# Kernel tuning notes

Measured on AMD Instinct MI355X. Metric: run time of the kernel, lower is better.

Reference implementation:

```python
import jax, jax.numpy as jnp
import numpy as np

B, S, H, NH = 2, 2048, 768, 12
HD = H // NH  # 64
MAXPOS = 2048


def _rope_tables(max_pos, d):
    # bert4torch get_sinusoid_encoding_table: even cols sin, odd cols cos
    pos = np.arange(max_pos, dtype=np.float32)[:, None]
    div = np.exp(np.arange(0, d, 2, dtype=np.float32) * (-np.log(10000.0) / d))
    tab = np.zeros((max_pos, d), np.float32)
    tab[:, 0::2] = np.sin(pos * div)
    tab[:, 1::2] = np.cos(pos * div)
    cos = np.concatenate([tab[:, 1::2], tab[:, 1::2]], axis=1)  # [:,1::2].repeat(1,2)
    sin = np.concatenate([tab[:, 0::2], tab[:, 0::2]], axis=1)  # [:,0::2].repeat(1,2)
    return jnp.asarray(cos), jnp.asarray(sin)


def setup_inputs() -> dict:
    key = jax.random.key(0)
    ks = jax.random.split(key, 10)
    s = 0.02
    inp = {}
    inp["hidden_states"] = jax.random.normal(ks[0], (B, S, H), jnp.float32)
    inp["attention_mask"] = jnp.ones((B, 1, 1, S), jnp.float32)
    for i, n in enumerate(["q", "k", "v", "o"]):
        inp[f"W{n}"] = (jax.random.normal(ks[1 + i], (H, H), jnp.float32) * s)
        inp[f"b{n}"] = jnp.zeros((H,), jnp.float32)
    cos, sin = _rope_tables(MAXPOS, HD)
    inp["cos_position"] = cos
    inp["sin_position"] = sin
    return inp


def _apply_rope(qw, cos, sin):
    # Faithful to source: seq_len_dim defaults to 1, which on a
    # [B, heads, S, head_dim] tensor is the HEADS axis.
    L = qw.shape[1]
    qw2 = jnp.concatenate([-qw[..., 1::2], qw[..., 0::2]], axis=-1)
    return qw * cos[:L][None, :, None, :] + qw2 * sin[:L][None, :, None, :]


def reference(hidden_states, attention_mask, Wq, bq, Wk, bk, Wv, bv, Wo, bo,
              cos_position, sin_position):
    b, s, _ = hidden_states.shape

    def heads(x):  # [b,s,H] -> [b,NH,s,HD]
        return x.reshape(b, s, NH, HD).transpose(0, 2, 1, 3)

    q = heads(hidden_states @ Wq + bq)
    k = heads(hidden_states @ Wk + bk)
    v = heads(hidden_states @ Wv + bv)
    q = _apply_rope(q, cos_position, sin_position)
    k = _apply_rope(k, cos_position, sin_position)
    scores = jnp.einsum('bnid,bnjd->bnij', q, k) / jnp.sqrt(jnp.float32(HD))
    scores = scores + (1.0 - attention_mask) * (-10000.0)
    probs = jax.nn.softmax(scores, axis=-1)  # dropout is identity in eval
    ctx = jnp.einsum('bnij,bnjd->bnid', probs, v)
    ctx = ctx.transpose(0, 2, 1, 3).reshape(b, s, H)
    return ctx @ Wo + bo
```

## Files before the change

### kernel.cpp

```cpp
#include <hip/hip_runtime.h>

#define B 2
#define S 2048
#define H 768
#define NH 12
#define HD 64
#define BS (B * S)
#define LOG2E 1.4426950408889634f

typedef unsigned short u16;
typedef short short8 __attribute__((ext_vector_type(8)));
typedef float f32x4 __attribute__((ext_vector_type(4)));

__device__ __forceinline__ u16 f2bf(float f) {
    union { float f; unsigned u; } c; c.f = f;
    unsigned u = c.u + 0x7FFFu + ((c.u >> 16) & 1u);
    return (u16)(u >> 16);
}
__device__ __forceinline__ float bf2f(u16 h) {
    union { unsigned u; float f; } c; c.u = ((unsigned)h) << 16;
    return c.f;
}

__device__ __forceinline__ void g2l16(const u16* g, u16* l) {
    __builtin_amdgcn_global_load_lds(
        (const __attribute__((address_space(1))) void*)g,
        (__attribute__((address_space(3))) void*)l, 16, 0, 0);
}

__global__ __launch_bounds__(256) void prep_hs_kernel(
    const float* __restrict__ src, u16* __restrict__ dst)
{
    size_t i = ((size_t)blockIdx.x * 256 + threadIdx.x) * 8;
    float4 a = *(const float4*)(src + i);
    float4 b = *(const float4*)(src + i + 4);
    short8 p;
    p[0] = (short)f2bf(a.x); p[1] = (short)f2bf(a.y);
    p[2] = (short)f2bf(a.z); p[3] = (short)f2bf(a.w);
    p[4] = (short)f2bf(b.x); p[5] = (short)f2bf(b.y);
    p[6] = (short)f2bf(b.z); p[7] = (short)f2bf(b.w);
    *(short8*)(dst + i) = p;
}

__global__ __launch_bounds__(256) void prep_w_kernel(
    const float* __restrict__ Wq, const float* __restrict__ Wk,
    const float* __restrict__ Wv, const float* __restrict__ Wo,
    u16* __restrict__ WTqkv, u16* __restrict__ WTo)
{
    __shared__ float Lt[64 * 65];
    const int t = threadIdx.x;
    const int z = blockIdx.z;
    const float* W = (z == 0) ? Wq : (z == 1) ? Wk : (z == 2) ? Wv : Wo;
    u16* D = (z == 3) ? WTo : (WTqkv + (size_t)z * H * H);
    const int k0 = blockIdx.x * 64, n0 = blockIdx.y * 64;

    #pragma unroll
    for (int u = 0; u < 4; ++u) {
        int f = t + u * 256;
        int r = f >> 4, c4 = (f & 15) * 4;
        float4 w = *(const float4*)(W + (size_t)(k0 + r) * H + n0 + c4);
        Lt[r * 65 + c4 + 0] = w.x; Lt[r * 65 + c4 + 1] = w.y;
        Lt[r * 65 + c4 + 2] = w.z; Lt[r * 65 + c4 + 3] = w.w;
    }
    __syncthreads();
    #pragma unroll
    for (int u = 0; u < 4; ++u) {
        int f = t + u * 256;
        int n = f >> 4, k4 = (f & 15) * 4;
        ushort4 p;
        p.x = f2bf(Lt[(k4 + 0) * 65 + n]);
        p.y = f2bf(Lt[(k4 + 1) * 65 + n]);
        p.z = f2bf(Lt[(k4 + 2) * 65 + n]);
        p.w = f2bf(Lt[(k4 + 3) * 65 + n]);
        *(ushort4*)(D + (size_t)(n0 + n) * H + k0 + k4) = p;
    }
}

__global__ __launch_bounds__(256) void gemm_qkv_kernel(
    const u16* __restrict__ A, const u16* __restrict__ BT,
    const float* __restrict__ bq, const float* __restrict__ bk,
    const float* __restrict__ bv,
    u16* __restrict__ Qb, u16* __restrict__ Kb, u16* __restrict__ VT)
{
    __shared__ alignas(16) u16 As[128 * 72];
    __shared__ alignas(16) u16 Bs[128 * 72];

    const int tid  = threadIdx.x;
    const int w    = tid >> 6;
    const int lane = tid & 63;
    const int quad = lane >> 4;
    const int l15  = lane & 15;
    const int wm = (w & 1) * 64, wn = (w >> 1) * 64;
    const int m0 = blockIdx.x * 128;
    const int n0 = blockIdx.y * 128;
    const int lr = tid >> 3, lc8 = (tid & 7) * 8;

    f32x4 acc[4][4];
    #pragma unroll
    for (int i = 0; i < 4; ++i)
        #pragma unroll
        for (int j = 0; j < 4; ++j) acc[i][j] = (f32x4){0.f, 0.f, 0.f, 0.f};

    short8 pa[2], pb[2], pa2[2], pb2[2];
    #pragma unroll
    for (int u = 0; u < 2; ++u) {
        pa[u]  = *(const short8*)(A  + (size_t)(m0 + lr + u * 32) * H + lc8);
        pb[u]  = *(const short8*)(BT + (size_t)(n0 + lr + u * 32) * H + lc8);
        pa2[u] = *(const short8*)(A  + (size_t)(m0 + lr + 64 + u * 32) * H + lc8);
        pb2[u] = *(const short8*)(BT + (size_t)(n0 + lr + 64 + u * 32) * H + lc8);
    }

    for (int k0 = 0; k0 < H; k0 += 64) {
        __syncthreads();
        #pragma unroll
        for (int u = 0; u < 2; ++u) {
            *(short8*)&As[(lr + u * 32) * 72 + lc8] = pa[u];
            *(short8*)&Bs[(lr + u * 32) * 72 + lc8] = pb[u];
            *(short8*)&As[(lr + 64 + u * 32) * 72 + lc8] = pa2[u];
            *(short8*)&Bs[(lr + 64 + u * 32) * 72 + lc8] = pb2[u];
        }
        if (k0 + 64 < H) {
            #pragma unroll
            for (int u = 0; u < 2; ++u) {
                pa[u]  = *(const short8*)(A  + (size_t)(m0 + lr + u * 32) * H + k0 + 64 + lc8);
                pb[u]  = *(const short8*)(BT + (size_t)(n0 + lr + u * 32) * H + k0 + 64 + lc8);
                pa2[u] = *(const short8*)(A  + (size_t)(m0 + lr + 64 + u * 32) * H + k0 + 64 + lc8);
                pb2[u] = *(const short8*)(BT + (size_t)(n0 + lr + 64 + u * 32) * H + k0 + 64 + lc8);
            }
        }
        __syncthreads();
        #pragma unroll
        for (int kc = 0; kc < 64; kc += 32) {
            short8 af[4], bf[4];
            #pragma unroll
            for (int mi = 0; mi < 4; ++mi)
                af[mi] = *(const short8*)&As[(wm + mi * 16 + l15) * 72 + kc + quad * 8];
            #pragma unroll
            for (int ni = 0; ni < 4; ++ni)
                bf[ni] = *(const short8*)&Bs[(wn + ni * 16 + l15) * 72 + kc + quad * 8];
            #pragma unroll
            for (int mi = 0; mi < 4; ++mi)
                #pragma unroll
                for (int ni = 0; ni < 4; ++ni)
                    acc[mi][ni] = __builtin_amdgcn_mfma_f32_16x16x32_bf16(
                        af[mi], bf[ni], acc[mi][ni], 0, 0, 0);
        }
    }

    #pragma unroll
    for (int mi = 0; mi < 4; ++mi) {
        const int mbase = m0 + wm + mi * 16 + quad * 4;
        #pragma unroll
        for (int ni = 0; ni < 4; ++ni) {
            const int col = n0 + wn + ni * 16 + l15;
            const int which = col / H;
            const int c = col - which * H;
            const int h = c >> 6, d = c & 63;
            if (which == 2) {
                const float bias = bv[c];
                const int b_ = mbase >> 11, s = mbase & (S - 1);
                ushort4 pk;
                pk.x = f2bf(acc[mi][ni][0] + bias);
                pk.y = f2bf(acc[mi][ni][1] + bias);
                pk.z = f2bf(acc[mi][ni][2] + bias);
                pk.w = f2bf(acc[mi][ni][3] + bias);
                *(ushort4*)&VT[(((size_t)b_ * NH + h) * HD + d) * S + s] = pk;
            } else {
                u16* dst = (which == 0) ? Qb : Kb;
                const float bias = (which == 0) ? bq[c] : bk[c];
                #pragma unroll
                for (int r = 0; r < 4; ++r) {
                    int m = mbase + r;
                    int b_ = m >> 11, s = m & (S - 1);
                    dst[(((size_t)b_ * NH + h) * S + s) * HD + d] =
                        f2bf(acc[mi][ni][r] + bias);
                }
            }
        }
    }
}

__global__ __launch_bounds__(256) void gemm_out_kernel(
    const u16* __restrict__ A, const u16* __restrict__ BT,
    const float* __restrict__ bo, float* __restrict__ out)
{
    __shared__ alignas(16) u16 As[128 * 72];
    __shared__ alignas(16) u16 Bs[128 * 72];

    const int tid  = threadIdx.x;
    const int w    = tid >> 6;
    const int lane = tid & 63;
    const int quad = lane >> 4;
    const int l15  = lane & 15;
    const int wm = (w & 1) * 64, wn = (w >> 1) * 64;
    const int m0 = blockIdx.x * 128;
    const int n0 = blockIdx.y * 128;
    const int lr = tid >> 3, lc8 = (tid & 7) * 8;

    f32x4 acc[4][4];
    #pragma unroll
    for (int i = 0; i < 4; ++i)
        #pragma unroll
        for (int j = 0; j < 4; ++j) acc[i][j] = (f32x4){0.f, 0.f, 0.f, 0.f};

    short8 pa[2], pb[2], pa2[2], pb2[2];
    #pragma unroll
    for (int u = 0; u < 2; ++u) {
        pa[u]  = *(const short8*)(A  + (size_t)(m0 + lr + u * 32) * H + lc8);
        pb[u]  = *(const short8*)(BT + (size_t)(n0 + lr + u * 32) * H + lc8);
        pa2[u] = *(const short8*)(A  + (size_t)(m0 + lr + 64 + u * 32) * H + lc8);
        pb2[u] = *(const short8*)(BT + (size_t)(n0 + lr + 64 + u * 32) * H + lc8);
    }

    for (int k0 = 0; k0 < H; k0 += 64) {
        __syncthreads();
        #pragma unroll
        for (int u = 0; u < 2; ++u) {
            *(short8*)&As[(lr + u * 32) * 72 + lc8] = pa[u];
            *(short8*)&Bs[(lr + u * 32) * 72 + lc8] = pb[u];
            *(short8*)&As[(lr + 64 + u * 32) * 72 + lc8] = pa2[u];
            *(short8*)&Bs[(lr + 64 + u * 32) * 72 + lc8] = pb2[u];
        }
        if (k0 + 64 < H) {
            #pragma unroll
            for (int u = 0; u < 2; ++u) {
                pa[u]  = *(const short8*)(A  + (size_t)(m0 + lr + u * 32) * H + k0 + 64 + lc8);
                pb[u]  = *(const short8*)(BT + (size_t)(n0 + lr + u * 32) * H + k0 + 64 + lc8);
                pa2[u] = *(const short8*)(A  + (size_t)(m0 + lr + 64 + u * 32) * H + k0 + 64 + lc8);
                pb2[u] = *(const short8*)(BT + (size_t)(n0 + lr + 64 + u * 32) * H + k0 + 64 + lc8);
            }
        }
        __syncthreads();
        #pragma unroll
        for (int kc = 0; kc < 64; kc += 32) {
            short8 af[4], bf[4];
            #pragma unroll
            for (int mi = 0; mi < 4; ++mi)
                af[mi] = *(const short8*)&As[(wm + mi * 16 + l15) * 72 + kc + quad * 8];
            #pragma unroll
            for (int ni = 0; ni < 4; ++ni)
                bf[ni] = *(const short8*)&Bs[(wn + ni * 16 + l15) * 72 + kc + quad * 8];
            #pragma unroll
            for (int mi = 0; mi < 4; ++mi)
                #pragma unroll
                for (int ni = 0; ni < 4; ++ni)
                    acc[mi][ni] = __builtin_amdgcn_mfma_f32_16x16x32_bf16(
                        af[mi], bf[ni], acc[mi][ni], 0, 0, 0);
        }
    }

    #pragma unroll
    for (int mi = 0; mi < 4; ++mi) {
        const int mbase = m0 + wm + mi * 16 + quad * 4;
        #pragma unroll
        for (int ni = 0; ni < 4; ++ni) {
            const int col = n0 + wn + ni * 16 + l15;
            const float bias = bo[col];
            #pragma unroll
            for (int r = 0; r < 4; ++r)
                out[(size_t)(mbase + r) * H + col] = acc[mi][ni][r] + bias;
        }
    }
}

__global__ __launch_bounds__(256) void rope_kernel(
    u16* __restrict__ Qb, u16* __restrict__ Kb,
    const float* __restrict__ cosp, const float* __restrict__ sinp)
{
    int row  = blockIdx.x * 4 + (threadIdx.x >> 6);
    int lane = threadIdx.x & 63;
    u16* X = (blockIdx.y == 0) ? Qb : Kb;
    const float scale = (blockIdx.y == 0) ? (0.125f * LOG2E) : 1.0f;
    int n = (row / S) % NH;
    float x = bf2f(X[(size_t)row * HD + lane]);
    int p = (lane < 32) ? (2 * lane + 1) : (2 * (lane - 32));
    float xp = __shfl(x, p, 64);
    float x2 = (lane < 32) ? -xp : xp;
    float c  = cosp[n * HD + lane];
    float sn = sinp[n * HD + lane];
    X[(size_t)row * HD + lane] = f2bf(fmaf(x, c, x2 * sn) * scale);
}

__global__ __launch_bounds__(256) void attn_mfma_kernel(
    const u16* __restrict__ Q, const u16* __restrict__ K,
    const u16* __restrict__ VT, const float* __restrict__ mask,
    u16* __restrict__ ctx)
{
    __shared__ alignas(16) u16 Kbuf[2][64 * 64];
    __shared__ alignas(16) u16 Vbuf[2][64 * 64];
    __shared__ alignas(16) u16 Ps[4 * 16 * 72];
    __shared__ float mt[S];

    const int tid  = threadIdx.x;
    const int w    = tid >> 6;
    const int lane = tid & 63;
    const int quad = lane >> 4;
    const int l15  = lane & 15;
    const int bn = blockIdx.y, b = bn / NH, hh = bn % NH;
    const int q0 = blockIdx.x * 64;
    const int NT = S / 64;

    {
        const float* mb = mask + (size_t)b * S;
        #pragma unroll
        for (int u = 0; u < 2; ++u) {
            int j = (tid + u * 256) * 4;
            float4 mv = *(const float4*)(mb + j);
            mt[j + 0] = (1.0f - mv.x) * (-10000.0f * LOG2E);
            mt[j + 1] = (1.0f - mv.y) * (-10000.0f * LOG2E);
            mt[j + 2] = (1.0f - mv.z) * (-10000.0f * LOG2E);
            mt[j + 3] = (1.0f - mv.w) * (-10000.0f * LOG2E);
        }
    }

    const u16* Qp = Q + ((size_t)bn * S + q0 + w * 16 + l15) * HD + quad * 8;
    const short8 qa0 = *(const short8*)(Qp);
    const short8 qa1 = *(const short8*)(Qp + 32);

    const u16* Kb = K + (size_t)bn * S * HD;
    const u16* Vb = VT + (size_t)bn * HD * S;

    int srow[2], slc[2];
    #pragma unroll
    for (int u = 0; u < 2; ++u) {
        int s = u * 256 + tid;
        srow[u] = s >> 3;
        slc[u]  = (s & 7) ^ (srow[u] & 7);
    }

    #define STAGE(JT, NB)                                                     \
        _Pragma("unroll")                                                     \
        for (int u = 0; u < 2; ++u) {                                         \
            g2l16(Kb + (size_t)((JT) * 64 + srow[u]) * HD + slc[u] * 8,       \
                  &Kbuf[NB][(u * 256 + w * 64) * 8]);                         \
            g2l16(Vb + (size_t)srow[u] * S + (JT) * 64 + slc[u] * 8,          \
                  &Vbuf[NB][(u * 256 + w * 64) * 8]);                         \
        }

    STAGE(0, 0)

    f32x4 o[4];
    float l_p[4];
    #pragma unroll
    for (int n = 0; n < 4; ++n) o[n] = (f32x4){0.f, 0.f, 0.f, 0.f};
    #pragma unroll
    for (int r = 0; r < 4; ++r) l_p[r] = 0.f;

    for (int jt = 0; jt < NT; ++jt) {
        const int cur = jt & 1;
        __syncthreads();
        if (jt + 1 < NT) { STAGE(jt + 1, cur ^ 1) }

        const u16* Kc = Kbuf[cur];
        const u16* Vc = Vbuf[cur];

        f32x4 sc[4];
        #pragma unroll
        for (int n = 0; n < 4; ++n) {
            const int row = n * 16 + l15, sw = row & 7;
            const short8 kb0 = *(const short8*)&Kc[row * 64 + ((quad) ^ sw) * 8];
            const short8 kb1 = *(const short8*)&Kc[row * 64 + ((quad + 4) ^ sw) * 8];
            f32x4 a = (f32x4){0.f, 0.f, 0.f, 0.f};
            a = __builtin_amdgcn_mfma_f32_16x16x32_bf16(qa0, kb0, a, 0, 0, 0);
            a = __builtin_amdgcn_mfma_f32_16x16x32_bf16(qa1, kb1, a, 0, 0, 0);
            sc[n] = a;
        }

        short8 vf[8];
        #pragma unroll
        for (int n = 0; n < 4; ++n) {
            const int row = n * 16 + l15, sw = row & 7;
            vf[n * 2 + 0] = *(const short8*)&Vc[row * 64 + ((quad) ^ sw) * 8];
            vf[n * 2 + 1] = *(const short8*)&Vc[row * 64 + ((quad + 4) ^ sw) * 8];
        }

        #pragma unroll
        for (int n = 0; n < 4; ++n) {
            const float mtn = mt[jt * 64 + n * 16 + l15];
            #pragma unroll
            for (int r = 0; r < 4; ++r) {
                float p = __builtin_amdgcn_exp2f(sc[n][r] + mtn);
                l_p[r] += p;
                Ps[w * 1152 + (quad * 4 + r) * 72 + n * 16 + l15] = f2bf(p);
            }
        }

        asm volatile("s_waitcnt lgkmcnt(0)" ::: "memory");

        const u16* Pw = &Ps[w * 1152 + l15 * 72 + quad * 8];
        const short8 pa0 = *(const short8*)(Pw);
        const short8 pa1 = *(const short8*)(Pw + 32);
        #pragma unroll
        for (int n = 0; n < 4; ++n) {
            o[n] = __builtin_amdgcn_mfma_f32_16x16x32_bf16(pa0, vf[n * 2 + 0], o[n], 0, 0, 0);
            o[n] = __builtin_amdgcn_mfma_f32_16x16x32_bf16(pa1, vf[n * 2 + 1], o[n], 0, 0, 0);
        }
    }
    #undef STAGE

    #pragma unroll
    for (int r = 0; r < 4; ++r) {
        float l = l_p[r];
        #pragma unroll
        for (int off = 8; off >= 1; off >>= 1)
            l += __shfl_xor(l, off, 16);
        float inv = 1.0f / l;
        int s = q0 + w * 16 + quad * 4 + r;
        #pragma unroll
        for (int n = 0; n < 4; ++n)
            ctx[((size_t)b * S + s) * H + hh * 64 + n * 16 + l15] =
                f2bf(o[n][r] * inv);
    }
}

extern "C" void kernel_launch(void* const* d_in, const int* in_sizes, int n_in,
                              void* d_out, int out_size, void* d_ws, size_t ws_size,
                              hipStream_t stream)
{
    const float* hs   = (const float*)d_in[0];
    const float* mask = (const float*)d_in[1];
    const float* Wq   = (const float*)d_in[2];
    const float* bq   = (const float*)d_in[3];
    const float* Wk   = (const float*)d_in[4];
    const float* bk   = (const float*)d_in[5];
    const float* Wv   = (const float*)d_in[6];
    const float* bv   = (const float*)d_in[7];
    const float* Wo   = (const float*)d_in[8];
    const float* bo   = (const float*)d_in[9];
    const float* cosp = (const float*)d_in[10];
    const float* sinp = (const float*)d_in[11];
    float* out = (float*)d_out;

    const size_t per = (size_t)B * NH * S * HD;
    u16* ws    = (u16*)d_ws;
    u16* hsb   = ws;
    u16* WTqkv = hsb + per;
    u16* WTo   = WTqkv + (size_t)3 * H * H;
    u16* Qb    = WTo + (size_t)H * H;
    u16* Kb    = Qb + per;
    u16* VT    = Kb + per;
    u16* ctxb  = VT + per;

    prep_hs_kernel<<<(BS * H) / 2048, 256, 0, stream>>>(hs, hsb);
    prep_w_kernel<<<dim3(12, 12, 4), 256, 0, stream>>>(
        Wq, Wk, Wv, Wo, WTqkv, WTo);

    gemm_qkv_kernel<<<dim3(BS / 128, 2304 / 128), 256, 0, stream>>>(
        hsb, WTqkv, bq, bk, bv, Qb, Kb, VT);

    rope_kernel<<<dim3(B * NH * S / 4, 2), 256, 0, stream>>>(
        Qb, Kb, cosp, sinp);

    attn_mfma_kernel<<<dim3(S / 64, B * NH), 256, 0, stream>>>(
        Qb, Kb, VT, mask, ctxb);

    gemm_out_kernel<<<dim3(BS / 128, H / 128), 256, 0, stream>>>(
        ctxb, WTo, bo, out);
}
```

Measured before the change: 206.8 us.

## Use 2 waves with 32 query rows each in attention; halve output GEMM N tile

```diff
diff --git a/kernel.cpp b/kernel.cpp
--- a/kernel.cpp
+++ b/kernel.cpp
@@ -185,31 +185,30 @@
     const float* __restrict__ bo, float* __restrict__ out)
 {
     __shared__ alignas(16) u16 As[128 * 72];
-    __shared__ alignas(16) u16 Bs[128 * 72];
+    __shared__ alignas(16) u16 Bs[64 * 72];
 
     const int tid  = threadIdx.x;
     const int w    = tid >> 6;
     const int lane = tid & 63;
     const int quad = lane >> 4;
     const int l15  = lane & 15;
-    const int wm = (w & 1) * 64, wn = (w >> 1) * 64;
+    const int wm = (w & 1) * 64, wn = (w >> 1) * 32;
     const int m0 = blockIdx.x * 128;
-    const int n0 = blockIdx.y * 128;
+    const int n0 = blockIdx.y * 64;
     const int lr = tid >> 3, lc8 = (tid & 7) * 8;
 
-    f32x4 acc[4][4];
+    f32x4 acc[4][2];
     #pragma unroll
     for (int i = 0; i < 4; ++i)
         #pragma unroll
-        for (int j = 0; j < 4; ++j) acc[i][j] = (f32x4){0.f, 0.f, 0.f, 0.f};
-
-    short8 pa[2], pb[2], pa2[2], pb2[2];
+        for (int j = 0; j < 2; ++j) acc[i][j] = (f32x4){0.f, 0.f, 0.f, 0.f};
+
+    short8 pa[2], pa2[2], pb[2];
     #pragma unroll
     for (int u = 0; u < 2; ++u) {
         pa[u]  = *(const short8*)(A  + (size_t)(m0 + lr + u * 32) * H + lc8);
+        pa2[u] = *(const short8*)(A  + (size_t)(m0 + lr + 64 + u * 32) * H + lc8);
         pb[u]  = *(const short8*)(BT + (size_t)(n0 + lr + u * 32) * H + lc8);
-        pa2[u] = *(const short8*)(A  + (size_t)(m0 + lr + 64 + u * 32) * H + lc8);
-        pb2[u] = *(const short8*)(BT + (size_t)(n0 + lr + 64 + u * 32) * H + lc8);
     }
 
     for (int k0 = 0; k0 < H; k0 += 64) {
@@ -217,33 +216,31 @@
         #pragma unroll
         for (int u = 0; u < 2; ++u) {
             *(short8*)&As[(lr + u * 32) * 72 + lc8] = pa[u];
+            *(short8*)&As[(lr + 64 + u * 32) * 72 + lc8] = pa2[u];
             *(short8*)&Bs[(lr + u * 32) * 72 + lc8] = pb[u];
-            *(short8*)&As[(lr + 64 + u * 32) * 72 + lc8] = pa2[u];
-            *(short8*)&Bs[(lr + 64 + u * 32) * 72 + lc8] = pb2[u];
         }
         if (k0 + 64 < H) {
             #pragma unroll
             for (int u = 0; u < 2; ++u) {
                 pa[u]  = *(const short8*)(A  + (size_t)(m0 + lr + u * 32) * H + k0 + 64 + lc8);
+                pa2[u] = *(const short8*)(A  + (size_t)(m0 + lr + 64 + u * 32) * H + k0 + 64 + lc8);
                 pb[u]  = *(const short8*)(BT + (size_t)(n0 + lr + u * 32) * H + k0 + 64 + lc8);
-                pa2[u] = *(const short8*)(A  + (size_t)(m0 + lr + 64 + u * 32) * H + k0 + 64 + lc8);
-                pb2[u] = *(const short8*)(BT + (size_t)(n0 + lr + 64 + u * 32) * H + k0 + 64 + lc8);
             }
         }
         __syncthreads();
         #pragma unroll
         for (int kc = 0; kc < 64; kc += 32) {
-            short8 af[4], bf[4];
+            short8 af[4], bf[2];
             #pragma unroll
             for (int mi = 0; mi < 4; ++mi)
                 af[mi] = *(const short8*)&As[(wm + mi * 16 + l15) * 72 + kc + quad * 8];
             #pragma unroll
-            for (int ni = 0; ni < 4; ++ni)
+            for (int ni = 0; ni < 2; ++ni)
                 bf[ni] = *(const short8*)&Bs[(wn + ni * 16 + l15) * 72 + kc + quad * 8];
             #pragma unroll
             for (int mi = 0; mi < 4; ++mi)
                 #pragma unroll
-                for (int ni = 0; ni < 4; ++ni)
+                for (int ni = 0; ni < 2; ++ni)
                     acc[mi][ni] = __builtin_amdgcn_mfma_f32_16x16x32_bf16(
                         af[mi], bf[ni], acc[mi][ni], 0, 0, 0);
         }
@@ -253,7 +250,7 @@
     for (int mi = 0; mi < 4; ++mi) {
         const int mbase = m0 + wm + mi * 16 + quad * 4;
         #pragma unroll
-        for (int ni = 0; ni < 4; ++ni) {
+        for (int ni = 0; ni < 2; ++ni) {
             const int col = n0 + wn + ni * 16 + l15;
             const float bias = bo[col];
             #pragma unroll
@@ -281,14 +278,14 @@
     X[(size_t)row * HD + lane] = f2bf(fmaf(x, c, x2 * sn) * scale);
 }
 
-__global__ __launch_bounds__(256) void attn_mfma_kernel(
+__global__ __launch_bounds__(128) void attn_mfma_kernel(
     const u16* __restrict__ Q, const u16* __restrict__ K,
     const u16* __restrict__ VT, const float* __restrict__ mask,
     u16* __restrict__ ctx)
 {
     __shared__ alignas(16) u16 Kbuf[2][64 * 64];
     __shared__ alignas(16) u16 Vbuf[2][64 * 64];
-    __shared__ alignas(16) u16 Ps[4 * 16 * 72];
+    __shared__ alignas(16) u16 Ps[2 * 32 * 72];
     __shared__ float mt[S];
 
     const int tid  = threadIdx.x;
@@ -303,8 +300,8 @@
     {
         const float* mb = mask + (size_t)b * S;
         #pragma unroll
-        for (int u = 0; u < 2; ++u) {
-            int j = (tid + u * 256) * 4;
+        for (int u = 0; u < 4; ++u) {
+            int j = (u * 128 + tid) * 4;
             float4 mv = *(const float4*)(mb + j);
             mt[j + 0] = (1.0f - mv.x) * (-10000.0f * LOG2E);
             mt[j + 1] = (1.0f - mv.y) * (-10000.0f * LOG2E);
@@ -313,38 +310,46 @@
         }
     }
 
-    const u16* Qp = Q + ((size_t)bn * S + q0 + w * 16 + l15) * HD + quad * 8;
-    const short8 qa0 = *(const short8*)(Qp);
-    const short8 qa1 = *(const short8*)(Qp + 32);
+    short8 qa[2][2];
+    #pragma unroll
+    for (int t = 0; t < 2; ++t) {
+        const u16* Qp =
+            Q + ((size_t)bn * S + q0 + w * 32 + t * 16 + l15) * HD + quad * 8;
+        qa[t][0] = *(const short8*)(Qp);
+        qa[t][1] = *(const short8*)(Qp + 32);
+    }
 
     const u16* Kb = K + (size_t)bn * S * HD;
     const u16* Vb = VT + (size_t)bn * HD * S;
 
-    int srow[2], slc[2];
-    #pragma unroll
-    for (int u = 0; u < 2; ++u) {
-        int s = u * 256 + tid;
+    int srow[4], slc[4];
+    #pragma unroll
+    for (int u = 0; u < 4; ++u) {
+        int s = u * 128 + tid;
         srow[u] = s >> 3;
         slc[u]  = (s & 7) ^ (srow[u] & 7);
     }
 
     #define STAGE(JT, NB)                                                     \
         _Pragma("unroll")                                                     \
-        for (int u = 0; u < 2; ++u) {                                         \
+        for (int u = 0; u < 4; ++u) {                                         \
             g2l16(Kb + (size_t)((JT) * 64 + srow[u]) * HD + slc[u] * 8,       \
-                  &Kbuf[NB][(u * 256 + w * 64) * 8]);                         \
+                  &Kbuf[NB][(u * 128 + w * 64) * 8]);                         \
             g2l16(Vb + (size_t)srow[u] * S + (JT) * 64 + slc[u] * 8,          \
-                  &Vbuf[NB][(u * 256 + w * 64) * 8]);                         \
+                  &Vbuf[NB][(u * 128 + w * 64) * 8]);                         \
         }
 
     STAGE(0, 0)
 
-    f32x4 o[4];
-    float l_p[4];
-    #pragma unroll
-    for (int n = 0; n < 4; ++n) o[n] = (f32x4){0.f, 0.f, 0.f, 0.f};
-    #pragma unroll
-    for (int r = 0; r < 4; ++r) l_p[r] = 0.f;
+    f32x4 o[2][4];
+    float l_p[2][4];
+    #pragma unroll
+    for (int t = 0; t < 2; ++t)
+        #pragma unroll
+        for (int n = 0; n < 4; ++n) {
+            o[t][n] = (f32x4){0.f, 0.f, 0.f, 0.f};
+            l_p[t][n] = 0.f;
+        }
 
     for (int jt = 0; jt < NT; ++jt) {
         const int cur = jt & 1;
@@ -354,63 +359,79 @@
         const u16* Kc = Kbuf[cur];
         const u16* Vc = Vbuf[cur];
 
-        f32x4 sc[4];
+        f32x4 sc[2][4];
         #pragma unroll
         for (int n = 0; n < 4; ++n) {
             const int row = n * 16 + l15, sw = row & 7;
             const short8 kb0 = *(const short8*)&Kc[row * 64 + ((quad) ^ sw) * 8];
             const short8 kb1 = *(const short8*)&Kc[row * 64 + ((quad + 4) ^ sw) * 8];
-            f32x4 a = (f32x4){0.f, 0.f, 0.f, 0.f};
-            a = __builtin_amdgcn_mfma_f32_16x16x32_bf16(qa0, kb0, a, 0, 0, 0);
-            a = __builtin_amdgcn_mfma_f32_16x16x32_bf16(qa1, kb1, a, 0, 0, 0);
-            sc[n] = a;
-        }
-
-        short8 vf[8];
+            #pragma unroll
+            for (int t = 0; t < 2; ++t) {
+                f32x4 a = (f32x4){0.f, 0.f, 0.f, 0.f};
+                a = __builtin_amdgcn_mfma_f32_16x16x32_bf16(qa[t][0], kb0, a, 0, 0, 0);
+                a = __builtin_amdgcn_mfma_f32_16x16x32_bf16(qa[t][1], kb1, a, 0, 0, 0);
+                sc[t][n] = a;
+            }
+        }
+
+        short8 vf[4][2];
         #pragma unroll
         for (int n = 0; n < 4; ++n) {
             const int row = n * 16 + l15, sw = row & 7;
-            vf[n * 2 + 0] = *(const short8*)&Vc[row * 64 + ((quad) ^ sw) * 8];
-            vf[n * 2 + 1] = *(const short8*)&Vc[row * 64 + ((quad + 4) ^ sw) * 8];
+            vf[n][0] = *(const short8*)&Vc[row * 64 + ((quad) ^ sw) * 8];
+            vf[n][1] = *(const short8*)&Vc[row * 64 + ((quad + 4) ^ sw) * 8];
         }
 
         #pragma unroll
         for (int n = 0; n < 4; ++n) {
             const float mtn = mt[jt * 64 + n * 16 + l15];
             #pragma unroll
-            for (int r = 0; r < 4; ++r) {
-                float p = __builtin_amdgcn_exp2f(sc[n][r] + mtn);
-                l_p[r] += p;
-                Ps[w * 1152 + (quad * 4 + r) * 72 + n * 16 + l15] = f2bf(p);
+            for (int t = 0; t < 2; ++t)
+                #pragma unroll
+                for (int r = 0; r < 4; ++r) {
+                    float p = __builtin_amdgcn_exp2f(sc[t][n][r] + mtn);
+                    l_p[t][r] += p;
+                    Ps[w * 2304 + (t * 16 + quad * 4 + r) * 72 + n * 16 + l15] =
+                        f2bf(p);
+                }
+        }
+
+        asm volatile("s_waitcnt lgkmcnt(0)" ::: "memory");
+
+        short8 pa[2][2];
+        #pragma unroll
+        for (int t = 0; t < 2; ++t) {
+            const u16* Pw = &Ps[w * 2304 + (t * 16 + l15) * 72 + quad * 8];
+            pa[t][0] = *(const short8*)(Pw);
+            pa[t][1] = *(const short8*)(Pw + 32);
+        }
+        #pragma unroll
+        for (int n = 0; n < 4; ++n)
+            #pragma unroll
+            for (int t = 0; t < 2; ++t) {
+                o[t][n] = __builtin_amdgcn_mfma_f32_16x16x32_bf16(
+                    pa[t][0], vf[n][0], o[t][n], 0, 0, 0);
+                o[t][n] = __builtin_amdgcn_mfma_f32_16x16x32_bf16(
+                    pa[t][1], vf[n][1], o[t][n], 0, 0, 0);
             }
-        }
-
-        asm volatile("s_waitcnt lgkmcnt(0)" ::: "memory");
-
-        const u16* Pw = &Ps[w * 1152 + l15 * 72 + quad * 8];
-        const short8 pa0 = *(const short8*)(Pw);
-        const short8 pa1 = *(const short8*)(Pw + 32);
-        #pragma unroll
-        for (int n = 0; n < 4; ++n) {
-            o[n] = __builtin_amdgcn_mfma_f32_16x16x32_bf16(pa0, vf[n * 2 + 0], o[n], 0, 0, 0);
-            o[n] = __builtin_amdgcn_mfma_f32_16x16x32_bf16(pa1, vf[n * 2 + 1], o[n], 0, 0, 0);
-        }
     }
     #undef STAGE
 
     #pragma unroll
-    for (int r = 0; r < 4; ++r) {
-        float l = l_p[r];
-        #pragma unroll
-        for (int off = 8; off >= 1; off >>= 1)
-            l += __shfl_xor(l, off, 16);
-        float inv = 1.0f / l;
-        int s = q0 + w * 16 + quad * 4 + r;
-        #pragma unroll
-        for (int n = 0; n < 4; ++n)
-            ctx[((size_t)b * S + s) * H + hh * 64 + n * 16 + l15] =
-                f2bf(o[n][r] * inv);
-    }
+    for (int t = 0; t < 2; ++t)
+        #pragma unroll
+        for (int r = 0; r < 4; ++r) {
+            float l = l_p[t][r];
+            #pragma unroll
+            for (int off = 8; off >= 1; off >>= 1)
+                l += __shfl_xor(l, off, 16);
+            float inv = 1.0f / l;
+            int s = q0 + w * 32 + t * 16 + quad * 4 + r;
+            #pragma unroll
+            for (int n = 0; n < 4; ++n)
+                ctx[((size_t)b * S + s) * H + hh * 64 + n * 16 + l15] =
+                    f2bf(o[t][n][r] * inv);
+        }
 }
 
 extern "C" void kernel_launch(void* const* d_in, const int* in_sizes, int n_in,
@@ -451,9 +472,9 @@
     rope_kernel<<<dim3(B * NH * S / 4, 2), 256, 0, stream>>>(
         Qb, Kb, cosp, sinp);
 
-    attn_mfma_kernel<<<dim3(S / 64, B * NH), 256, 0, stream>>>(
+    attn_mfma_kernel<<<dim3(S / 64, B * NH), 128, 0, stream>>>(
         Qb, Kb, VT, mask, ctxb);
 
-    gemm_out_kernel<<<dim3(BS / 128, H / 128), 256, 0, stream>>>(
+    gemm_out_kernel<<<dim3(BS / 128, H / 64), 256, 0, stream>>>(
         ctxb, WTo, bo, out);
 }
```

Result: slower. 217.3 us (+5.1%).

## Use 32x32 MFMA with split-K waves in attention; halve output GEMM N tile

Applied to the files above, without the earlier changes.

```diff
diff --git a/kernel.cpp b/kernel.cpp
--- a/kernel.cpp
+++ b/kernel.cpp
@@ -11,6 +11,7 @@
 typedef unsigned short u16;
 typedef short short8 __attribute__((ext_vector_type(8)));
 typedef float f32x4 __attribute__((ext_vector_type(4)));
+typedef float f32x16 __attribute__((ext_vector_type(16)));
 
 __device__ __forceinline__ u16 f2bf(float f) {
     union { float f; unsigned u; } c; c.f = f;
@@ -20,6 +21,12 @@
 __device__ __forceinline__ float bf2f(u16 h) {
     union { unsigned u; float f; } c; c.u = ((unsigned)h) << 16;
     return c.f;
+}
+__device__ __forceinline__ f32x16 zero16() {
+    f32x16 v;
+    #pragma unroll
+    for (int i = 0; i < 16; ++i) v[i] = 0.f;
+    return v;
 }
 
 __device__ __forceinline__ void g2l16(const u16* g, u16* l) {
@@ -185,31 +192,30 @@
     const float* __restrict__ bo, float* __restrict__ out)
 {
     __shared__ alignas(16) u16 As[128 * 72];
-    __shared__ alignas(16) u16 Bs[128 * 72];
+    __shared__ alignas(16) u16 Bs[64 * 72];
 
     const int tid  = threadIdx.x;
     const int w    = tid >> 6;
     const int lane = tid & 63;
     const int quad = lane >> 4;
     const int l15  = lane & 15;
-    const int wm = (w & 1) * 64, wn = (w >> 1) * 64;
+    const int wm = (w & 1) * 64, wn = (w >> 1) * 32;
     const int m0 = blockIdx.x * 128;
-    const int n0 = blockIdx.y * 128;
+    const int n0 = blockIdx.y * 64;
     const int lr = tid >> 3, lc8 = (tid & 7) * 8;
 
-    f32x4 acc[4][4];
+    f32x4 acc[4][2];
     #pragma unroll
     for (int i = 0; i < 4; ++i)
         #pragma unroll
-        for (int j = 0; j < 4; ++j) acc[i][j] = (f32x4){0.f, 0.f, 0.f, 0.f};
-
-    short8 pa[2], pb[2], pa2[2], pb2[2];
+        for (int j = 0; j < 2; ++j) acc[i][j] = (f32x4){0.f, 0.f, 0.f, 0.f};
+
+    short8 pa[2], pa2[2], pb[2];
     #pragma unroll
     for (int u = 0; u < 2; ++u) {
         pa[u]  = *(const short8*)(A  + (size_t)(m0 + lr + u * 32) * H + lc8);
+        pa2[u] = *(const short8*)(A  + (size_t)(m0 + lr + 64 + u * 32) * H + lc8);
         pb[u]  = *(const short8*)(BT + (size_t)(n0 + lr + u * 32) * H + lc8);
-        pa2[u] = *(const short8*)(A  + (size_t)(m0 + lr + 64 + u * 32) * H + lc8);
-        pb2[u] = *(const short8*)(BT + (size_t)(n0 + lr + 64 + u * 32) * H + lc8);
     }
 
     for (int k0 = 0; k0 < H; k0 += 64) {
@@ -217,33 +223,31 @@
         #pragma unroll
         for (int u = 0; u < 2; ++u) {
             *(short8*)&As[(lr + u * 32) * 72 + lc8] = pa[u];
+            *(short8*)&As[(lr + 64 + u * 32) * 72 + lc8] = pa2[u];
             *(short8*)&Bs[(lr + u * 32) * 72 + lc8] = pb[u];
-            *(short8*)&As[(lr + 64 + u * 32) * 72 + lc8] = pa2[u];
-            *(short8*)&Bs[(lr + 64 + u * 32) * 72 + lc8] = pb2[u];
         }
         if (k0 + 64 < H) {
             #pragma unroll
             for (int u = 0; u < 2; ++u) {
                 pa[u]  = *(const short8*)(A  + (size_t)(m0 + lr + u * 32) * H + k0 + 64 + lc8);
+                pa2[u] = *(const short8*)(A  + (size_t)(m0 + lr + 64 + u * 32) * H + k0 + 64 + lc8);
                 pb[u]  = *(const short8*)(BT + (size_t)(n0 + lr + u * 32) * H + k0 + 64 + lc8);
-                pa2[u] = *(const short8*)(A  + (size_t)(m0 + lr + 64 + u * 32) * H + k0 + 64 + lc8);
-                pb2[u] = *(const short8*)(BT + (size_t)(n0 + lr + 64 + u * 32) * H + k0 + 64 + lc8);
             }
         }
         __syncthreads();
         #pragma unroll
         for (int kc = 0; kc < 64; kc += 32) {
-            short8 af[4], bf[4];
+            short8 af[4], bf[2];
             #pragma unroll
             for (int mi = 0; mi < 4; ++mi)
                 af[mi] = *(const short8*)&As[(wm + mi * 16 + l15) * 72 + kc + quad * 8];
             #pragma unroll
-            for (int ni = 0; ni < 4; ++ni)
+            for (int ni = 0; ni < 2; ++ni)
                 bf[ni] = *(const short8*)&Bs[(wn + ni * 16 + l15) * 72 + kc + quad * 8];
             #pragma unroll
             for (int mi = 0; mi < 4; ++mi)
                 #pragma unroll
-                for (int ni = 0; ni < 4; ++ni)
+                for (int ni = 0; ni < 2; ++ni)
                     acc[mi][ni] = __builtin_amdgcn_mfma_f32_16x16x32_bf16(
                         af[mi], bf[ni], acc[mi][ni], 0, 0, 0);
         }
@@ -253,7 +257,7 @@
     for (int mi = 0; mi < 4; ++mi) {
         const int mbase = m0 + wm + mi * 16 + quad * 4;
         #pragma unroll
-        for (int ni = 0; ni < 4; ++ni) {
+        for (int ni = 0; ni < 2; ++ni) {
             const int col = n0 + wn + ni * 16 + l15;
             const float bias = bo[col];
             #pragma unroll
@@ -286,39 +290,33 @@
     const u16* __restrict__ VT, const float* __restrict__ mask,
     u16* __restrict__ ctx)
 {
-    __shared__ alignas(16) u16 Kbuf[2][64 * 64];
-    __shared__ alignas(16) u16 Vbuf[2][64 * 64];
-    __shared__ alignas(16) u16 Ps[4 * 16 * 72];
-    __shared__ float mt[S];
+    __shared__ alignas(16) u16 smem[21504];
+    u16* const Kbase = smem;
+    u16* const Vbase = smem + 8192;
+    u16* const Psw   = smem + 16384 + (threadIdx.x >> 6) * 1280;
 
     const int tid  = threadIdx.x;
     const int w    = tid >> 6;
     const int lane = tid & 63;
-    const int quad = lane >> 4;
-    const int l15  = lane & 15;
+    const int l31  = lane & 31;
+    const int h5   = lane >> 5;
+    const int rh   = w & 1;
+    const int kh   = w >> 1;
     const int bn = blockIdx.y, b = bn / NH, hh = bn % NH;
     const int q0 = blockIdx.x * 64;
     const int NT = S / 64;
 
+    short8 qa[4];
     {
-        const float* mb = mask + (size_t)b * S;
-        #pragma unroll
-        for (int u = 0; u < 2; ++u) {
-            int j = (tid + u * 256) * 4;
-            float4 mv = *(const float4*)(mb + j);
-            mt[j + 0] = (1.0f - mv.x) * (-10000.0f * LOG2E);
-            mt[j + 1] = (1.0f - mv.y) * (-10000.0f * LOG2E);
-            mt[j + 2] = (1.0f - mv.z) * (-10000.0f * LOG2E);
-            mt[j + 3] = (1.0f - mv.w) * (-10000.0f * LOG2E);
-        }
-    }
-
-    const u16* Qp = Q + ((size_t)bn * S + q0 + w * 16 + l15) * HD + quad * 8;
-    const short8 qa0 = *(const short8*)(Qp);
-    const short8 qa1 = *(const short8*)(Qp + 32);
-
-    const u16* Kb = K + (size_t)bn * S * HD;
-    const u16* Vb = VT + (size_t)bn * HD * S;
+        const u16* Qp = Q + ((size_t)bn * S + q0 + rh * 32 + l31) * HD + h5 * 8;
+        #pragma unroll
+        for (int kc = 0; kc < 4; ++kc)
+            qa[kc] = *(const short8*)(Qp + kc * 16);
+    }
+
+    const u16* Kg = K + (size_t)bn * S * HD;
+    const u16* Vg = VT + (size_t)bn * HD * S;
+    const float* mrow = mask + (size_t)b * S;
 
     int srow[2], slc[2];
     #pragma unroll
@@ -331,85 +329,107 @@
     #define STAGE(JT, NB)                                                     \
         _Pragma("unroll")                                                     \
         for (int u = 0; u < 2; ++u) {                                         \
-            g2l16(Kb + (size_t)((JT) * 64 + srow[u]) * HD + slc[u] * 8,       \
-                  &Kbuf[NB][(u * 256 + w * 64) * 8]);                         \
-            g2l16(Vb + (size_t)srow[u] * S + (JT) * 64 + slc[u] * 8,          \
-                  &Vbuf[NB][(u * 256 + w * 64) * 8]);                         \
+            g2l16(Kg + (size_t)((JT) * 64 + srow[u]) * HD + slc[u] * 8,       \
+                  Kbase + (NB) * 4096 + (u * 256 + w * 64) * 8);              \
+            g2l16(Vg + (size_t)srow[u] * S + (JT) * 64 + slc[u] * 8,          \
+                  Vbase + (NB) * 4096 + (u * 256 + w * 64) * 8);              \
         }
 
     STAGE(0, 0)
 
-    f32x4 o[4];
-    float l_p[4];
-    #pragma unroll
-    for (int n = 0; n < 4; ++n) o[n] = (f32x4){0.f, 0.f, 0.f, 0.f};
-    #pragma unroll
-    for (int r = 0; r < 4; ++r) l_p[r] = 0.f;
+    f32x16 o0 = zero16(), o1 = zero16();
+    float l_p[16];
+    #pragma unroll
+    for (int i = 0; i < 16; ++i) l_p[i] = 0.f;
 
     for (int jt = 0; jt < NT; ++jt) {
         const int cur = jt & 1;
+        const float mv = mrow[jt * 64 + kh * 32 + l31];
         __syncthreads();
         if (jt + 1 < NT) { STAGE(jt + 1, cur ^ 1) }
 
-        const u16* Kc = Kbuf[cur];
-        const u16* Vc = Vbuf[cur];
-
-        f32x4 sc[4];
-        #pragma unroll
-        for (int n = 0; n < 4; ++n) {
-            const int row = n * 16 + l15, sw = row & 7;
-            const short8 kb0 = *(const short8*)&Kc[row * 64 + ((quad) ^ sw) * 8];
-            const short8 kb1 = *(const short8*)&Kc[row * 64 + ((quad + 4) ^ sw) * 8];
-            f32x4 a = (f32x4){0.f, 0.f, 0.f, 0.f};
-            a = __builtin_amdgcn_mfma_f32_16x16x32_bf16(qa0, kb0, a, 0, 0, 0);
-            a = __builtin_amdgcn_mfma_f32_16x16x32_bf16(qa1, kb1, a, 0, 0, 0);
-            sc[n] = a;
-        }
-
-        short8 vf[8];
-        #pragma unroll
-        for (int n = 0; n < 4; ++n) {
-            const int row = n * 16 + l15, sw = row & 7;
-            vf[n * 2 + 0] = *(const short8*)&Vc[row * 64 + ((quad) ^ sw) * 8];
-            vf[n * 2 + 1] = *(const short8*)&Vc[row * 64 + ((quad + 4) ^ sw) * 8];
-        }
-
-        #pragma unroll
-        for (int n = 0; n < 4; ++n) {
-            const float mtn = mt[jt * 64 + n * 16 + l15];
-            #pragma unroll
-            for (int r = 0; r < 4; ++r) {
-                float p = __builtin_amdgcn_exp2f(sc[n][r] + mtn);
-                l_p[r] += p;
-                Ps[w * 1152 + (quad * 4 + r) * 72 + n * 16 + l15] = f2bf(p);
+        const u16* Kc = Kbase + cur * 4096;
+        const u16* Vc = Vbase + cur * 4096;
+
+        f32x16 sc = zero16();
+        {
+            const int krow = kh * 32 + l31;
+            const int sw = krow & 7;
+            #pragma unroll
+            for (int kc = 0; kc < 4; ++kc) {
+                const short8 kb =
+                    *(const short8*)&Kc[krow * 64 + ((kc * 2 + h5) ^ sw) * 8];
+                sc = __builtin_amdgcn_mfma_f32_32x32x16_bf16(qa[kc], kb, sc, 0, 0, 0);
             }
         }
 
+        const float mt = (1.0f - mv) * (-10000.0f * LOG2E);
+        #pragma unroll
+        for (int reg = 0; reg < 16; ++reg) {
+            float p = __builtin_amdgcn_exp2f(sc[reg] + mt);
+            l_p[reg] += p;
+            const int r32 = (reg & 3) + 8 * (reg >> 2) + 4 * h5;
+            Psw[r32 * 40 + l31] = f2bf(p);
+        }
+
         asm volatile("s_waitcnt lgkmcnt(0)" ::: "memory");
 
-        const u16* Pw = &Ps[w * 1152 + l15 * 72 + quad * 8];
-        const short8 pa0 = *(const short8*)(Pw);
-        const short8 pa1 = *(const short8*)(Pw + 32);
-        #pragma unroll
-        for (int n = 0; n < 4; ++n) {
-            o[n] = __builtin_amdgcn_mfma_f32_16x16x32_bf16(pa0, vf[n * 2 + 0], o[n], 0, 0, 0);
-            o[n] = __builtin_amdgcn_mfma_f32_16x16x32_bf16(pa1, vf[n * 2 + 1], o[n], 0, 0, 0);
+        const short8 pa0 = *(const short8*)&Psw[l31 * 40 + h5 * 8];
+        const short8 pa1 = *(const short8*)&Psw[l31 * 40 + 16 + h5 * 8];
+
+        #pragma unroll
+        for (int nt = 0; nt < 2; ++nt) {
+            const int vrow = nt * 32 + l31;
+            const int sw = vrow & 7;
+            const short8 vb0 =
+                *(const short8*)&Vc[vrow * 64 + ((kh * 4 + h5) ^ sw) * 8];
+            const short8 vb1 =
+                *(const short8*)&Vc[vrow * 64 + ((kh * 4 + 2 + h5) ^ sw) * 8];
+            f32x16& o = nt ? o1 : o0;
+            o = __builtin_amdgcn_mfma_f32_32x32x16_bf16(pa0, vb0, o, 0, 0, 0);
+            o = __builtin_amdgcn_mfma_f32_32x32x16_bf16(pa1, vb1, o, 0, 0, 0);
         }
     }
     #undef STAGE
 
     #pragma unroll
-    for (int r = 0; r < 4; ++r) {
-        float l = l_p[r];
-        #pragma unroll
-        for (int off = 8; off >= 1; off >>= 1)
-            l += __shfl_xor(l, off, 16);
-        float inv = 1.0f / l;
-        int s = q0 + w * 16 + quad * 4 + r;
-        #pragma unroll
-        for (int n = 0; n < 4; ++n)
-            ctx[((size_t)b * S + s) * H + hh * 64 + n * 16 + l15] =
-                f2bf(o[n][r] * inv);
+    for (int reg = 0; reg < 16; ++reg) {
+        #pragma unroll
+        for (int off = 16; off >= 1; off >>= 1)
+            l_p[reg] += __shfl_xor(l_p[reg], off, 32);
+    }
+
+    __syncthreads();
+    float* cb = (float*)smem;
+    float* lb = (float*)(smem + 16384);
+
+    if (kh == 1) {
+        float* c = cb + rh * 2048;
+        #pragma unroll
+        for (int reg = 0; reg < 16; ++reg) {
+            float2 v = make_float2(o0[reg], o1[reg]);
+            *(float2*)&c[reg * 128 + lane * 2] = v;
+        }
+        if (l31 == 0) {
+            #pragma unroll
+            for (int reg = 0; reg < 16; ++reg)
+                lb[rh * 32 + h5 * 16 + reg] = l_p[reg];
+        }
+    }
+    __syncthreads();
+    if (kh == 0) {
+        const float* c = cb + rh * 2048;
+        #pragma unroll
+        for (int reg = 0; reg < 16; ++reg) {
+            float2 po = *(const float2*)&c[reg * 128 + lane * 2];
+            float lt = l_p[reg] + lb[rh * 32 + h5 * 16 + reg];
+            float inv = 1.0f / lt;
+            const int r32 = (reg & 3) + 8 * (reg >> 2) + 4 * h5;
+            const int s = q0 + rh * 32 + r32;
+            u16* dst = ctx + ((size_t)b * S + s) * H + hh * 64;
+            dst[l31]      = f2bf((o0[reg] + po.x) * inv);
+            dst[32 + l31] = f2bf((o1[reg] + po.y) * inv);
+        }
     }
 }
 
@@ -454,6 +474,6 @@
     attn_mfma_kernel<<<dim3(S / 64, B * NH), 256, 0, stream>>>(
         Qb, Kb, VT, mask, ctxb);
 
-    gemm_out_kernel<<<dim3(BS / 128, H / 128), 256, 0, stream>>>(
+    gemm_out_kernel<<<dim3(BS / 128, H / 64), 256, 0, stream>>>(
         ctxb, WTo, bo, out);
 }
```

Measured after the change: 200.9 us. 2.8% less time.
